# Performance work log

Measured on AMD Instinct MI355X. Metric: run time of the kernel, lower is better.

The kernel has to match this reference:

```python
import jax, jax.numpy as jnp
import numpy as np

N_HEAD = 4
D_K = 64
D_V = 64
D_MODEL = 256
LN_EPS = 1e-5


def setup_inputs() -> dict:
    key = jax.random.key(0)
    k1, k2, k3 = jax.random.split(key, 3)
    B, C, H, W = 2, D_MODEL, 64, 64
    q = jax.random.normal(k1, (B, C, H, W), dtype=jnp.float32)
    # w_qkvs: Linear(d_model, n_head*d_k, bias=False), weight [out, in]
    std_qkv = np.sqrt(2.0 / (D_MODEL + D_K))
    w_qkv = jax.random.normal(k2, (N_HEAD * D_K, D_MODEL), dtype=jnp.float32) * std_qkv
    # fc: Linear(n_head*d_v, d_model), xavier-normal-ish init
    std_fc = np.sqrt(2.0 / (N_HEAD * D_V + D_MODEL))
    fc_w = jax.random.normal(k3, (D_MODEL, N_HEAD * D_V), dtype=jnp.float32) * std_fc
    fc_b = jnp.zeros((D_MODEL,), dtype=jnp.float32)
    ln_g = jnp.ones((D_MODEL,), dtype=jnp.float32)
    ln_b = jnp.zeros((D_MODEL,), dtype=jnp.float32)
    return {"q": q, "w_qkv": w_qkv, "fc_w": fc_w, "fc_b": fc_b, "ln_g": ln_g, "ln_b": ln_b}


def reference(q, w_qkv, fc_w, fc_b, ln_g, ln_b):
    B, C, H, W = q.shape
    L = H * W
    # [B, C, H, W] -> [B, L, C]
    x = q.reshape(B, C, L).transpose(0, 2, 1)
    residual = x
    # shared QKV projection (self-attention branch: q == k == v)
    qkv = x @ w_qkv.T                                  # [B, L, nh*dk]
    qh = qkv.reshape(B, L, N_HEAD, D_K).transpose(2, 0, 1, 3)  # [h, B, L, dk]
    scale = jnp.asarray(np.sqrt(D_K), dtype=q.dtype)
    attn = jnp.einsum('hbqd,hbkd->hbqk', qh, qh) / scale       # [h, B, L, L]
    attn = jax.nn.softmax(attn, axis=-1)
    out = jnp.einsum('hbqk,hbkd->hbqd', attn, qh)              # [h, B, L, dv]
    # [h, B, L, dv] -> [B, L, h*dv]
    out = out.transpose(1, 2, 0, 3).reshape(B, L, N_HEAD * D_V)
    out = out @ fc_w.T + fc_b
    out = out + residual
    mu = jnp.mean(out, axis=-1, keepdims=True)
    var = jnp.mean(jnp.square(out - mu), axis=-1, keepdims=True)
    out = (out - mu) / jnp.sqrt(var + LN_EPS) * ln_g + ln_b
    # raw row-major view back to [B, C, H, W] (matches torch .view)
    return out.reshape(B, -1, H, W)
```

## Files before the change

kernel.cpp:

```cpp
#include <hip/hip_runtime.h>

#define L_SEQ 4096
#define DMODEL 256
#define DH 64

typedef __attribute__((ext_vector_type(8))) __bf16 bf16x8;
typedef __attribute__((ext_vector_type(4))) __bf16 bf16v4;
typedef __attribute__((ext_vector_type(8))) __bf16 bf16v8;
typedef __attribute__((ext_vector_type(4))) float f32x4;
typedef __attribute__((ext_vector_type(8))) float f32x8;
typedef __attribute__((ext_vector_type(8))) unsigned short ushort8v;
typedef __attribute__((ext_vector_type(4))) unsigned short ushort4v;

__device__ __forceinline__ float bf2f(unsigned short h) {
  unsigned u = ((unsigned)h) << 16;
  return __builtin_bit_cast(float, u);
}
__device__ __forceinline__ ushort4v cvt4(float a, float b, float c, float d) {
  bf16v4 h = __builtin_convertvector((f32x4){a, b, c, d}, bf16v4);
  return __builtin_bit_cast(ushort4v, h);
}
__device__ __forceinline__ ushort8v cvt8(f32x8 v) {
  bf16v8 h = __builtin_convertvector(v, bf16v8);
  return __builtin_bit_cast(ushort8v, h);
}
__device__ __forceinline__ unsigned short f2bf(float f) {
  __bf16 h = (__bf16)f;
  return __builtin_bit_cast(unsigned short, h);
}
__device__ __forceinline__ bf16x8 ld_frag(const unsigned short* p) {
  return __builtin_bit_cast(bf16x8, *(const ushort8v*)p);
}

#define KP2 136
__global__ __launch_bounds__(256) void k_qkv(const float* __restrict__ q,
                                             const float* __restrict__ w,
                                             unsigned short* __restrict__ Qh,
                                             unsigned short* __restrict__ QhT) {
  __shared__ unsigned short As[64 * KP2];
  __shared__ unsigned short Bs[64 * KP2];
  int bx = blockIdx.x;
  int mtile = bx >> 2, h = bx & 3;
  int m0 = mtile * 64;
  int b = m0 >> 12, l0 = m0 & 4095;
  int t = threadIdx.x;
  int wv = t >> 6, lane = t & 63, g = lane >> 4, ln = lane & 15;
  f32x4 acc[4] = {};
  for (int kb = 0; kb < 2; ++kb) {
#pragma unroll
    for (int it = 0; it < 8; ++it) {
      int idx = t + it * 256;
      int cl = idx & 127;
      int lq = idx >> 7;
      float4 v = *(const float4*)(q + ((size_t)(b * 256 + kb * 128 + cl)) * 4096 + l0 + lq * 4);
      As[(lq * 4 + 0) * KP2 + cl] = f2bf(v.x);
      As[(lq * 4 + 1) * KP2 + cl] = f2bf(v.y);
      As[(lq * 4 + 2) * KP2 + cl] = f2bf(v.z);
      As[(lq * 4 + 3) * KP2 + cl] = f2bf(v.w);
    }
#pragma unroll
    for (int it = 0; it < 4; ++it) {
      int idx = t + it * 256;
      int row = idx >> 4;
      int c8 = (idx & 15) * 8;
      const float* src = w + (size_t)(h * 64 + row) * 256 + kb * 128 + c8;
      float4 v0 = *(const float4*)(src);
      float4 v1 = *(const float4*)(src + 4);
      *(ushort8v*)(Bs + row * KP2 + c8) =
          cvt8((f32x8){v0.x, v0.y, v0.z, v0.w, v1.x, v1.y, v1.z, v1.w});
    }
    __syncthreads();
#pragma unroll
    for (int kc = 0; kc < 4; ++kc) {
      bf16x8 a = ld_frag(As + (wv * 16 + ln) * KP2 + kc * 32 + g * 8);
#pragma unroll
      for (int tn = 0; tn < 4; ++tn) {
        bf16x8 bb = ld_frag(Bs + (tn * 16 + ln) * KP2 + kc * 32 + g * 8);
        acc[tn] = __builtin_amdgcn_mfma_f32_16x16x32_bf16(a, bb, acc[tn], 0, 0, 0);
      }
    }
    __syncthreads();
  }
  size_t pbase = (size_t)(b * 4 + h);
#pragma unroll
  for (int tn = 0; tn < 4; ++tn) {
#pragma unroll
    for (int r = 0; r < 4; ++r) {
      int lrow = wv * 16 + g * 4 + r;
      int d = tn * 16 + ln;
      unsigned short bv = f2bf(acc[tn][r]);
      As[lrow * 64 + (((d >> 3) ^ (lrow & 7)) * 8) + (d & 7)] = bv;
      Bs[d * 64 + (((lrow >> 3) ^ (d & 7)) * 8) + (lrow & 7)] = bv;
    }
  }
#pragma unroll
  for (int s = 0; s < 2; ++s) {
    int flat = s * 64 + lane;
    int lrow = wv * 16 + (flat >> 3);
    int c8 = lane & 7;
    ushort8v v = *(const ushort8v*)(As + lrow * 64 + ((c8 ^ (lrow & 7)) * 8));
    *(ushort8v*)(Qh + (pbase * L_SEQ + l0 + lrow) * DH + c8 * 8) = v;
  }
  __syncthreads();
#pragma unroll
  for (int s = 0; s < 2; ++s) {
    int flat = s * 256 + t;
    int drow = flat >> 3;
    int c8 = t & 7;
    ushort8v v = *(const ushort8v*)(Bs + drow * 64 + ((c8 ^ (drow & 7)) * 8));
    *(ushort8v*)(QhT + (pbase * DH + drow) * L_SEQ + l0 + c8 * 8) = v;
  }
}

template <int KSPLIT>
__global__ __launch_bounds__(256, 2) void k_attn(const unsigned short* __restrict__ Qh,
                                                 const unsigned short* __restrict__ QhT,
                                                 unsigned short* __restrict__ Opart,
                                                 float* __restrict__ Lpart) {
  const int NKB = 64 / KSPLIT;
  __shared__ unsigned short Kt[64 * 64];
  __shared__ unsigned short Vt[64 * 64];
  __shared__ unsigned short Pb[256 * 64];
  int bx = blockIdx.x;
  int p = bx & 7;
  int u = bx >> 3;
  int qsup = u & 15, ks = u >> 4;
  int t = threadIdx.x;
  int wv = t >> 6, lane = t & 63, g = lane >> 4, ln = lane & 15;
  const unsigned short* Qp = Qh + (size_t)p * L_SEQ * DH;
  const unsigned short* QTp = QhT + (size_t)p * DH * L_SEQ;
  int q0 = qsup * 256;
  int qw = q0 + wv * 64;

  bf16x8 aQ[4][2];
#pragma unroll
  for (int nt = 0; nt < 4; ++nt)
#pragma unroll
    for (int kc = 0; kc < 2; ++kc)
      aQ[nt][kc] = ld_frag(Qp + (size_t)(qw + nt * 16 + ln) * DH + kc * 32 + g * 8);

  f32x4 oacc[4][4] = {};
  float lacc[4] = {0.f, 0.f, 0.f, 0.f};

  int srow0 = t >> 3, scol0 = t & 7;
  int srow1 = (t + 256) >> 3, scol1 = (t + 256) & 7;
  int sdst0 = srow0 * 64 + ((scol0 ^ (srow0 & 7)) * 8);
  int sdst1 = srow1 * 64 + ((scol1 ^ (srow1 & 7)) * 8);

  ushort8v kreg0, kreg1, vreg0, vreg1;
  {
    int kbase = (ks * NKB) * 64;
    kreg0 = *(const ushort8v*)(Qp + (size_t)(kbase + srow0) * DH + scol0 * 8);
    kreg1 = *(const ushort8v*)(Qp + (size_t)(kbase + srow1) * DH + scol1 * 8);
    vreg0 = *(const ushort8v*)(QTp + (size_t)srow0 * L_SEQ + kbase + scol0 * 8);
    vreg1 = *(const ushort8v*)(QTp + (size_t)srow1 * L_SEQ + kbase + scol1 * 8);
  }

  for (int kb = 0; kb < NKB; ++kb) {
    __syncthreads();
    *(ushort8v*)(Kt + sdst0) = kreg0;
    *(ushort8v*)(Kt + sdst1) = kreg1;
    *(ushort8v*)(Vt + sdst0) = vreg0;
    *(ushort8v*)(Vt + sdst1) = vreg1;
    __syncthreads();
    if (kb + 1 < NKB) {
      int kbase = (ks * NKB + kb + 1) * 64;
      kreg0 = *(const ushort8v*)(Qp + (size_t)(kbase + srow0) * DH + scol0 * 8);
      kreg1 = *(const ushort8v*)(Qp + (size_t)(kbase + srow1) * DH + scol1 * 8);
      vreg0 = *(const ushort8v*)(QTp + (size_t)srow0 * L_SEQ + kbase + scol0 * 8);
      vreg1 = *(const ushort8v*)(QTp + (size_t)srow1 * L_SEQ + kbase + scol1 * 8);
    }
#pragma unroll
    for (int mt = 0; mt < 4; ++mt) {
      int krow = mt * 16 + ln;
      bf16x8 aK0 = ld_frag(Kt + krow * 64 + (((0 * 4 + g) ^ (ln & 7)) * 8));
      bf16x8 aK1 = ld_frag(Kt + krow * 64 + (((1 * 4 + g) ^ (ln & 7)) * 8));
      f32x4 s[4] = {};
#pragma unroll
      for (int nt = 0; nt < 4; ++nt) {
        s[nt] = __builtin_amdgcn_mfma_f32_16x16x32_bf16(aK0, aQ[nt][0], s[nt], 0, 0, 0);
        s[nt] = __builtin_amdgcn_mfma_f32_16x16x32_bf16(aK1, aQ[nt][1], s[nt], 0, 0, 0);
      }
#pragma unroll
      for (int nt = 0; nt < 4; ++nt) {
        float p0 = __expf(fmaf(s[nt][0], 0.125f, -16.0f));
        float p1 = __expf(fmaf(s[nt][1], 0.125f, -16.0f));
        float p2 = __expf(fmaf(s[nt][2], 0.125f, -16.0f));
        float p3 = __expf(fmaf(s[nt][3], 0.125f, -16.0f));
        lacc[nt] += (p0 + p1) + (p2 + p3);
        ushort4v pk = cvt4(p0, p1, p2, p3);
        int row = wv * 64 + nt * 16 + ln;
        int addr = row * 64 + (((2 * mt + (g >> 1)) ^ (ln & 7)) * 8) + (g & 1) * 4;
        *(ushort4v*)(Pb + addr) = pk;
      }
    }
#pragma unroll
    for (int kc = 0; kc < 2; ++kc) {
      bf16x8 bV[4];
#pragma unroll
      for (int tn = 0; tn < 4; ++tn)
        bV[tn] = ld_frag(Vt + (tn * 16 + ln) * 64 + (((kc * 4 + g) ^ (ln & 7)) * 8));
#pragma unroll
      for (int mq = 0; mq < 4; ++mq) {
        bf16x8 aP = ld_frag(Pb + (wv * 64 + mq * 16 + ln) * 64 + (((kc * 4 + g) ^ (ln & 7)) * 8));
#pragma unroll
        for (int tn = 0; tn < 4; ++tn)
          oacc[mq][tn] = __builtin_amdgcn_mfma_f32_16x16x32_bf16(aP, bV[tn], oacc[mq][tn], 0, 0, 0);
      }
    }
  }
#pragma unroll
  for (int nt = 0; nt < 4; ++nt) {
    lacc[nt] += __shfl_xor(lacc[nt], 16, 64);
    lacc[nt] += __shfl_xor(lacc[nt], 32, 64);
  }
  size_t pq = (size_t)(ks * 8 + p) * L_SEQ;
  if (g == 0) {
#pragma unroll
    for (int nt = 0; nt < 4; ++nt)
      __builtin_nontemporal_store(lacc[nt], &Lpart[pq + qw + nt * 16 + ln]);
  }
#pragma unroll
  for (int mq = 0; mq < 4; ++mq) {
#pragma unroll
    for (int r = 0; r < 4; ++r) {
      int row = wv * 64 + mq * 16 + g * 4 + r;
#pragma unroll
      for (int tn = 0; tn < 4; ++tn) {
        int d = tn * 16 + ln;
        Pb[row * 64 + (((d >> 3) ^ (row & 7)) * 8) + (d & 7)] = f2bf(oacc[mq][tn][r]);
      }
    }
  }
#pragma unroll
  for (int s = 0; s < 8; ++s) {
    int flat = s * 64 + lane;
    int row = wv * 64 + (flat >> 3);
    int c8 = lane & 7;
    ushort8v v = *(const ushort8v*)(Pb + row * 64 + ((c8 ^ (row & 7)) * 8));
    __builtin_nontemporal_store(v, (ushort8v*)(Opart + (pq + q0 + row) * DH + c8 * 8));
  }
}

#define CP 72
template <int KSPLIT>
__global__ __launch_bounds__(256) void k_fc(const unsigned short* __restrict__ Opart,
                                            const float* __restrict__ Lpart,
                                            const float* __restrict__ fcw,
                                            const float* __restrict__ qres,
                                            const float* __restrict__ fcb,
                                            const float* __restrict__ lng,
                                            const float* __restrict__ lnb,
                                            float* __restrict__ out) {
  __shared__ unsigned short As[32 * CP];
  __shared__ unsigned short Bs[256 * CP];
  __shared__ float redS[4][32], redQ[4][32], muA[32], rsA[32];
  int bx = blockIdx.x;
  int m0 = bx * 32;
  int b = m0 >> 12, lpart = m0 & 4095;
  int t = threadIdx.x;
  int wv = t >> 6, lane = t & 63, g = lane >> 4, ln = lane & 15;
  f32x4 acc[2][4] = {};
  for (int kb = 0; kb < 4; ++kb) {
    {
      int row = t >> 3, c0 = (t & 7) * 8;
      int qrow = lpart + row;
      int p = b * 4 + kb;
      float lsum = 0.f;
#pragma unroll
      for (int ksp = 0; ksp < KSPLIT; ++ksp)
        lsum += __builtin_nontemporal_load(&Lpart[(size_t)(ksp * 8 + p) * L_SEQ + qrow]);
      float inv = 1.0f / lsum;
      float a8[8] = {0.f, 0.f, 0.f, 0.f, 0.f, 0.f, 0.f, 0.f};
#pragma unroll
      for (int ksp = 0; ksp < KSPLIT; ++ksp) {
        ushort8v v = __builtin_nontemporal_load(
            (const ushort8v*)(Opart + ((size_t)(ksp * 8 + p) * L_SEQ + qrow) * DH + c0));
#pragma unroll
        for (int j = 0; j < 8; ++j) a8[j] += bf2f(v[j]);
      }
      *(ushort8v*)(As + row * CP + c0) =
          cvt8((f32x8){a8[0] * inv, a8[1] * inv, a8[2] * inv, a8[3] * inv,
                       a8[4] * inv, a8[5] * inv, a8[6] * inv, a8[7] * inv});
    }
#pragma unroll
    for (int it = 0; it < 8; ++it) {
      int idx = t + it * 256;
      int row = idx >> 3, c0 = (idx & 7) * 8;
      const float* src = fcw + (size_t)row * 256 + kb * 64 + c0;
      float4 v0 = *(const float4*)(src);
      float4 v1 = *(const float4*)(src + 4);
      *(ushort8v*)(Bs + row * CP + c0) =
          cvt8((f32x8){v0.x, v0.y, v0.z, v0.w, v1.x, v1.y, v1.z, v1.w});
    }
    __syncthreads();
#pragma unroll
    for (int kc = 0; kc < 2; ++kc) {
      bf16x8 a[2], bb[4];
#pragma unroll
      for (int mt = 0; mt < 2; ++mt) a[mt] = ld_frag(As + (mt * 16 + ln) * CP + kc * 32 + g * 8);
#pragma unroll
      for (int tn = 0; tn < 4; ++tn) bb[tn] = ld_frag(Bs + (wv * 64 + tn * 16 + ln) * CP + kc * 32 + g * 8);
#pragma unroll
      for (int mt = 0; mt < 2; ++mt)
#pragma unroll
        for (int tn = 0; tn < 4; ++tn)
          acc[mt][tn] = __builtin_amdgcn_mfma_f32_16x16x32_bf16(a[mt], bb[tn], acc[mt][tn], 0, 0, 0);
    }
    __syncthreads();
  }
  float fb[4], lg[4], lb[4];
#pragma unroll
  for (int tn = 0; tn < 4; ++tn) {
    int o = wv * 64 + tn * 16 + ln;
    fb[tn] = fcb[o]; lg[tn] = lng[o]; lb[tn] = lnb[o];
  }
#pragma unroll
  for (int mt = 0; mt < 2; ++mt) {
    float ps[4] = {0.f, 0.f, 0.f, 0.f}, pq2[4] = {0.f, 0.f, 0.f, 0.f};
#pragma unroll
    for (int tn = 0; tn < 4; ++tn) {
      int o = wv * 64 + tn * 16 + ln;
      float4 res = *(const float4*)(qres + ((size_t)(b * 256 + o)) * 4096 + lpart + mt * 16 + g * 4);
      float rv[4] = {res.x, res.y, res.z, res.w};
#pragma unroll
      for (int r = 0; r < 4; ++r) {
        float v = acc[mt][tn][r] + fb[tn] + rv[r];
        acc[mt][tn][r] = v;
        ps[r] += v;
        pq2[r] += v * v;
      }
    }
#pragma unroll
    for (int r = 0; r < 4; ++r) {
      float s = ps[r], q2 = pq2[r];
#pragma unroll
      for (int off = 1; off < 16; off <<= 1) {
        s += __shfl_xor(s, off, 64);
        q2 += __shfl_xor(q2, off, 64);
      }
      if (ln == 0) {
        int row = mt * 16 + g * 4 + r;
        redS[wv][row] = s;
        redQ[wv][row] = q2;
      }
    }
  }
  __syncthreads();
  if (t < 32) {
    float s = redS[0][t] + redS[1][t] + redS[2][t] + redS[3][t];
    float q2 = redQ[0][t] + redQ[1][t] + redQ[2][t] + redQ[3][t];
    float mu = s * (1.f / 256.f);
    float var = q2 * (1.f / 256.f) - mu * mu;
    muA[t] = mu;
    rsA[t] = rsqrtf(var + 1e-5f);
  }
  __syncthreads();
#pragma unroll
  for (int mt = 0; mt < 2; ++mt) {
#pragma unroll
    for (int r = 0; r < 4; ++r) {
      int row = mt * 16 + g * 4 + r;
      float mu = muA[row], rs = rsA[row];
#pragma unroll
      for (int tn = 0; tn < 4; ++tn) {
        int o = wv * 64 + tn * 16 + ln;
        out[(size_t)(m0 + row) * 256 + o] = (acc[mt][tn][r] - mu) * rs * lg[tn] + lb[tn];
      }
    }
  }
}

extern "C" void kernel_launch(void* const* d_in, const int* in_sizes, int n_in,
                              void* d_out, int out_size, void* d_ws, size_t ws_size,
                              hipStream_t stream) {
  const float* q = (const float*)d_in[0];
  const float* w_qkv = (const float*)d_in[1];
  const float* fc_w = (const float*)d_in[2];
  const float* fc_b = (const float*)d_in[3];
  const float* ln_g = (const float*)d_in[4];
  const float* ln_b = (const float*)d_in[5];
  float* out = (float*)d_out;

  unsigned short* Qh = (unsigned short*)d_ws;
  unsigned short* QhT = Qh + 2097152;
  unsigned short* Opart = QhT + 2097152;

  size_t need8 = (size_t)2 * 2097152 * 2 + (size_t)8 * 8 * 4096 * 64 * 2 + (size_t)8 * 8 * 4096 * 4;

  k_qkv<<<dim3(512), dim3(256), 0, stream>>>(q, w_qkv, Qh, QhT);
  if (ws_size >= need8) {
    float* Lpart = (float*)(Opart + (size_t)8 * 8 * 4096 * 64);
    k_attn<8><<<dim3(1024), dim3(256), 0, stream>>>(Qh, QhT, Opart, Lpart);
    k_fc<8><<<dim3(256), dim3(256), 0, stream>>>(Opart, Lpart, fc_w, q, fc_b, ln_g, ln_b, out);
  } else {
    float* Lpart = (float*)(Opart + (size_t)4 * 8 * 4096 * 64);
    k_attn<4><<<dim3(512), dim3(256), 0, stream>>>(Qh, QhT, Opart, Lpart);
    k_fc<4><<<dim3(256), dim3(256), 0, stream>>>(Opart, Lpart, fc_w, q, fc_b, ln_g, ln_b, out);
  }
}
```

Measured before the change: 156.1 us.

## Add bf16 transpose pre-pass and halve fc row tile with hoisted softmax norms

Adds a separate kernel that transposes the input from channel-major to row-major bf16 through shared memory, so the QKV projection can load contiguous 16-byte vectors instead of doing scattered 2-byte shared stores. The fc/LayerNorm kernel now processes 16 rows per block instead of 32, which doubles the grid to 512 blocks, and it computes the softmax normalizers once per block up front. The workspace is reorganized so the transposed input reuses the Opart region and Lpart sits before it. The cost is an extra kernel launch and an extra round trip of the input through global memory. Only half the threads now take part in loading the A tile in the fc kernel.

```diff
diff --git a/kernel.cpp b/kernel.cpp
--- a/kernel.cpp
+++ b/kernel.cpp
@@ -32,8 +32,37 @@
   return __builtin_bit_cast(bf16x8, *(const ushort8v*)p);
 }
 
+__global__ __launch_bounds__(256) void k_transpose(const float* __restrict__ q,
+                                                   unsigned short* __restrict__ xbf) {
+  __shared__ float T[64 * 65];
+  int bx = blockIdx.x;
+  int b = bx >> 8, rest = bx & 255;
+  int ct = rest >> 6, lt = rest & 63;
+  int t = threadIdx.x;
+#pragma unroll
+  for (int it = 0; it < 4; ++it) {
+    int i = (t >> 4) + it * 16;
+    int j0 = (t & 15) * 4;
+    float4 v = *(const float4*)(q + ((size_t)(b * 256 + ct * 64 + i)) * 4096 + lt * 64 + j0);
+    T[i * 65 + j0 + 0] = v.x;
+    T[i * 65 + j0 + 1] = v.y;
+    T[i * 65 + j0 + 2] = v.z;
+    T[i * 65 + j0 + 3] = v.w;
+  }
+  __syncthreads();
+#pragma unroll
+  for (int it = 0; it < 2; ++it) {
+    int l = (t >> 3) + it * 32;
+    int c0 = (t & 7) * 8;
+    f32x8 v;
+#pragma unroll
+    for (int k = 0; k < 8; ++k) v[k] = T[(c0 + k) * 65 + l];
+    *(ushort8v*)(xbf + ((size_t)(b * 4096 + lt * 64 + l)) * 256 + ct * 64 + c0) = cvt8(v);
+  }
+}
+
 #define KP2 136
-__global__ __launch_bounds__(256) void k_qkv(const float* __restrict__ q,
+__global__ __launch_bounds__(256) void k_qkv(const unsigned short* __restrict__ xbf,
                                              const float* __restrict__ w,
                                              unsigned short* __restrict__ Qh,
                                              unsigned short* __restrict__ QhT) {
@@ -48,15 +77,12 @@
   f32x4 acc[4] = {};
   for (int kb = 0; kb < 2; ++kb) {
 #pragma unroll
-    for (int it = 0; it < 8; ++it) {
+    for (int it = 0; it < 4; ++it) {
       int idx = t + it * 256;
-      int cl = idx & 127;
-      int lq = idx >> 7;
-      float4 v = *(const float4*)(q + ((size_t)(b * 256 + kb * 128 + cl)) * 4096 + l0 + lq * 4);
-      As[(lq * 4 + 0) * KP2 + cl] = f2bf(v.x);
-      As[(lq * 4 + 1) * KP2 + cl] = f2bf(v.y);
-      As[(lq * 4 + 2) * KP2 + cl] = f2bf(v.z);
-      As[(lq * 4 + 3) * KP2 + cl] = f2bf(v.w);
+      int row = idx >> 4;
+      int c0 = (idx & 15) * 8;
+      *(ushort8v*)(As + row * KP2 + c0) =
+          *(const ushort8v*)(xbf + (size_t)(m0 + row) * 256 + kb * 128 + c0);
     }
 #pragma unroll
     for (int it = 0; it < 4; ++it) {
@@ -252,25 +278,32 @@
                                             const float* __restrict__ lng,
                                             const float* __restrict__ lnb,
                                             float* __restrict__ out) {
-  __shared__ unsigned short As[32 * CP];
+  __shared__ unsigned short As[16 * CP];
   __shared__ unsigned short Bs[256 * CP];
-  __shared__ float redS[4][32], redQ[4][32], muA[32], rsA[32];
+  __shared__ float invL[4][16];
+  __shared__ float redS[4][16], redQ[4][16], muA[16], rsA[16];
   int bx = blockIdx.x;
-  int m0 = bx * 32;
+  int m0 = bx * 16;
   int b = m0 >> 12, lpart = m0 & 4095;
   int t = threadIdx.x;
   int wv = t >> 6, lane = t & 63, g = lane >> 4, ln = lane & 15;
-  f32x4 acc[2][4] = {};
+  if (t < 64) {
+    int row = t >> 2, hh = t & 3;
+    int p = b * 4 + hh;
+    float lsum = 0.f;
+#pragma unroll
+    for (int ksp = 0; ksp < KSPLIT; ++ksp)
+      lsum += Lpart[(size_t)(ksp * 8 + p) * L_SEQ + lpart + row];
+    invL[hh][row] = 1.0f / lsum;
+  }
+  __syncthreads();
+  f32x4 acc[4] = {};
   for (int kb = 0; kb < 4; ++kb) {
-    {
+    if (t < 128) {
       int row = t >> 3, c0 = (t & 7) * 8;
       int qrow = lpart + row;
       int p = b * 4 + kb;
-      float lsum = 0.f;
-#pragma unroll
-      for (int ksp = 0; ksp < KSPLIT; ++ksp)
-        lsum += __builtin_nontemporal_load(&Lpart[(size_t)(ksp * 8 + p) * L_SEQ + qrow]);
-      float inv = 1.0f / lsum;
+      float inv = invL[kb][row];
       float a8[8] = {0.f, 0.f, 0.f, 0.f, 0.f, 0.f, 0.f, 0.f};
 #pragma unroll
       for (int ksp = 0; ksp < KSPLIT; ++ksp) {
@@ -296,16 +329,12 @@
     __syncthreads();
 #pragma unroll
     for (int kc = 0; kc < 2; ++kc) {
-      bf16x8 a[2], bb[4];
-#pragma unroll
-      for (int mt = 0; mt < 2; ++mt) a[mt] = ld_frag(As + (mt * 16 + ln) * CP + kc * 32 + g * 8);
-#pragma unroll
-      for (int tn = 0; tn < 4; ++tn) bb[tn] = ld_frag(Bs + (wv * 64 + tn * 16 + ln) * CP + kc * 32 + g * 8);
-#pragma unroll
-      for (int mt = 0; mt < 2; ++mt)
-#pragma unroll
-        for (int tn = 0; tn < 4; ++tn)
-          acc[mt][tn] = __builtin_amdgcn_mfma_f32_16x16x32_bf16(a[mt], bb[tn], acc[mt][tn], 0, 0, 0);
+      bf16x8 a = ld_frag(As + ln * CP + kc * 32 + g * 8);
+#pragma unroll
+      for (int tn = 0; tn < 4; ++tn) {
+        bf16x8 bb = ld_frag(Bs + (wv * 64 + tn * 16 + ln) * CP + kc * 32 + g * 8);
+        acc[tn] = __builtin_amdgcn_mfma_f32_16x16x32_bf16(a, bb, acc[tn], 0, 0, 0);
+      }
     }
     __syncthreads();
   }
@@ -315,39 +344,36 @@
     int o = wv * 64 + tn * 16 + ln;
     fb[tn] = fcb[o]; lg[tn] = lng[o]; lb[tn] = lnb[o];
   }
-#pragma unroll
-  for (int mt = 0; mt < 2; ++mt) {
-    float ps[4] = {0.f, 0.f, 0.f, 0.f}, pq2[4] = {0.f, 0.f, 0.f, 0.f};
-#pragma unroll
-    for (int tn = 0; tn < 4; ++tn) {
-      int o = wv * 64 + tn * 16 + ln;
-      float4 res = *(const float4*)(qres + ((size_t)(b * 256 + o)) * 4096 + lpart + mt * 16 + g * 4);
-      float rv[4] = {res.x, res.y, res.z, res.w};
-#pragma unroll
-      for (int r = 0; r < 4; ++r) {
-        float v = acc[mt][tn][r] + fb[tn] + rv[r];
-        acc[mt][tn][r] = v;
-        ps[r] += v;
-        pq2[r] += v * v;
-      }
-    }
+  float ps[4] = {0.f, 0.f, 0.f, 0.f}, pq2[4] = {0.f, 0.f, 0.f, 0.f};
+#pragma unroll
+  for (int tn = 0; tn < 4; ++tn) {
+    int o = wv * 64 + tn * 16 + ln;
+    float4 res = *(const float4*)(qres + ((size_t)(b * 256 + o)) * 4096 + lpart + g * 4);
+    float rv[4] = {res.x, res.y, res.z, res.w};
 #pragma unroll
     for (int r = 0; r < 4; ++r) {
-      float s = ps[r], q2 = pq2[r];
-#pragma unroll
-      for (int off = 1; off < 16; off <<= 1) {
-        s += __shfl_xor(s, off, 64);
-        q2 += __shfl_xor(q2, off, 64);
-      }
-      if (ln == 0) {
-        int row = mt * 16 + g * 4 + r;
-        redS[wv][row] = s;
-        redQ[wv][row] = q2;
-      }
+      float v = acc[tn][r] + fb[tn] + rv[r];
+      acc[tn][r] = v;
+      ps[r] += v;
+      pq2[r] += v * v;
+    }
+  }
+#pragma unroll
+  for (int r = 0; r < 4; ++r) {
+    float s = ps[r], q2 = pq2[r];
+#pragma unroll
+    for (int off = 1; off < 16; off <<= 1) {
+      s += __shfl_xor(s, off, 64);
+      q2 += __shfl_xor(q2, off, 64);
+    }
+    if (ln == 0) {
+      int row = g * 4 + r;
+      redS[wv][row] = s;
+      redQ[wv][row] = q2;
     }
   }
   __syncthreads();
-  if (t < 32) {
+  if (t < 16) {
     float s = redS[0][t] + redS[1][t] + redS[2][t] + redS[3][t];
     float q2 = redQ[0][t] + redQ[1][t] + redQ[2][t] + redQ[3][t];
     float mu = s * (1.f / 256.f);
@@ -357,16 +383,13 @@
   }
   __syncthreads();
 #pragma unroll
-  for (int mt = 0; mt < 2; ++mt) {
-#pragma unroll
-    for (int r = 0; r < 4; ++r) {
-      int row = mt * 16 + g * 4 + r;
-      float mu = muA[row], rs = rsA[row];
-#pragma unroll
-      for (int tn = 0; tn < 4; ++tn) {
-        int o = wv * 64 + tn * 16 + ln;
-        out[(size_t)(m0 + row) * 256 + o] = (acc[mt][tn][r] - mu) * rs * lg[tn] + lb[tn];
-      }
+  for (int r = 0; r < 4; ++r) {
+    int row = g * 4 + r;
+    float mu = muA[row], rs = rsA[row];
+#pragma unroll
+    for (int tn = 0; tn < 4; ++tn) {
+      int o = wv * 64 + tn * 16 + ln;
+      out[(size_t)(m0 + row) * 256 + o] = (acc[tn][r] - mu) * rs * lg[tn] + lb[tn];
     }
   }
 }
@@ -384,18 +407,19 @@
 
   unsigned short* Qh = (unsigned short*)d_ws;
   unsigned short* QhT = Qh + 2097152;
-  unsigned short* Opart = QhT + 2097152;
-
-  size_t need8 = (size_t)2 * 2097152 * 2 + (size_t)8 * 8 * 4096 * 64 * 2 + (size_t)8 * 8 * 4096 * 4;
-
-  k_qkv<<<dim3(512), dim3(256), 0, stream>>>(q, w_qkv, Qh, QhT);
+  float* Lpart = (float*)(QhT + 2097152);
+  unsigned short* Opart = (unsigned short*)((char*)Lpart + 1048576);
+  unsigned short* xbf = Opart;
+
+  size_t need8 = (size_t)2 * 2097152 * 2 + 1048576 + (size_t)8 * 8 * 4096 * 64 * 2;
+
+  k_transpose<<<dim3(512), dim3(256), 0, stream>>>(q, xbf);
+  k_qkv<<<dim3(512), dim3(256), 0, stream>>>(xbf, w_qkv, Qh, QhT);
   if (ws_size >= need8) {
-    float* Lpart = (float*)(Opart + (size_t)8 * 8 * 4096 * 64);
     k_attn<8><<<dim3(1024), dim3(256), 0, stream>>>(Qh, QhT, Opart, Lpart);
-    k_fc<8><<<dim3(256), dim3(256), 0, stream>>>(Opart, Lpart, fc_w, q, fc_b, ln_g, ln_b, out);
+    k_fc<8><<<dim3(512), dim3(256), 0, stream>>>(Opart, Lpart, fc_w, q, fc_b, ln_g, ln_b, out);
   } else {
-    float* Lpart = (float*)(Opart + (size_t)4 * 8 * 4096 * 64);
     k_attn<4><<<dim3(512), dim3(256), 0, stream>>>(Qh, QhT, Opart, Lpart);
-    k_fc<4><<<dim3(256), dim3(256), 0, stream>>>(Opart, Lpart, fc_w, q, fc_b, ln_g, ln_b, out);
-  }
-}
+    k_fc<4><<<dim3(512), dim3(256), 0, stream>>>(Opart, Lpart, fc_w, q, fc_b, ln_g, ln_b, out);
+  }
+}
```

New measurement: 146.3 us. -6.3%, faster.
